# Kernel optimization log

Hardware: AMD Instinct MI355X
Metric: run time of the kernel (lower is better)

Reference implementation:

```python
import jax, jax.numpy as jnp
import numpy as np


def _lstm_cell(x, h, c, Wih, Whh, b):
    # torch gate order: input, forget, cell(g), output
    gates = x @ Wih.T + h @ Whh.T + b  # [B, 4H]
    i, f, g, o = jnp.split(gates, 4, axis=-1)
    i = jax.nn.sigmoid(i)
    f = jax.nn.sigmoid(f)
    g = jnp.tanh(g)
    o = jax.nn.sigmoid(o)
    c = f * c + i * g
    return o * jnp.tanh(c), c


def setup_inputs() -> dict:
    key = jax.random.key(0)
    ks = jax.random.split(key, 20)
    B, Te, Td, X, H = 4096, 168, 24, 8, 64
    s = 0.1  # weight scale for numerical sanity in the AR sampling loop
    return {
        "enc_x": jax.random.normal(ks[0], (B, Te, X), jnp.float32),
        "enc_z": jax.random.uniform(ks[1], (B, Te, 1), jnp.float32),
        "dec_x": jax.random.normal(ks[2], (B, Td, X - 1), jnp.float32),
        "v": jax.random.uniform(ks[3], (B, 1, 1), jnp.float32) + 0.5,  # positive scale
        "eps": jax.random.normal(ks[4], (B, Td, 1), jnp.float32),
        "W_ih0": s * jax.random.normal(ks[5], (4 * H, X), jnp.float32),
        "W_hh0": s * jax.random.normal(ks[6], (4 * H, H), jnp.float32),
        "b0": s * jax.random.normal(ks[7], (4 * H,), jnp.float32),
        "W_ih1": s * jax.random.normal(ks[8], (4 * H, H), jnp.float32),
        "W_hh1": s * jax.random.normal(ks[9], (4 * H, H), jnp.float32),
        "b1": s * jax.random.normal(ks[10], (4 * H,), jnp.float32),
        "W_ih2": s * jax.random.normal(ks[11], (4 * H, H), jnp.float32),
        "W_hh2": s * jax.random.normal(ks[12], (4 * H, H), jnp.float32),
        "b2": s * jax.random.normal(ks[13], (4 * H,), jnp.float32),
        "w_m": s * jax.random.normal(ks[14], (H, 1), jnp.float32),
        "b_m": jnp.zeros((1,), jnp.float32),
        "w_a": s * jax.random.normal(ks[15], (H, 1), jnp.float32),
        "b_a": jnp.zeros((1,), jnp.float32),
    }


def reference(enc_x, enc_z, dec_x, v, eps,
              W_ih0, W_hh0, b0, W_ih1, W_hh1, b1, W_ih2, W_hh2, b2,
              w_m, b_m, w_a, b_a):
    B = enc_x.shape[0]
    H = W_hh0.shape[1]

    def step3(x, h, c):
        h0, c0 = _lstm_cell(x, h[0], c[0], W_ih0, W_hh0, b0)
        h1, c1 = _lstm_cell(h0, h[1], c[1], W_ih1, W_hh1, b1)
        h2, c2 = _lstm_cell(h1, h[2], c[2], W_ih2, W_hh2, b2)
        return (h0, h1, h2), (c0, c1, c2), h2

    z0 = jnp.zeros((B, H), enc_x.dtype)
    h = (z0, z0, z0)
    c = (z0, z0, z0)

    # ---- encoder: 3-layer LSTM over Te steps ----
    def enc_step(carry, x_t):
        h, c = carry
        h, c, _ = step3(x_t, h, c)
        return (h, c), None

    (h, c), _ = jax.lax.scan(enc_step, (h, c), jnp.swapaxes(enc_x, 0, 1))

    vf = v[:, 0, :]                 # [B, 1]
    z = enc_z[:, -1, :] / vf        # [B, 1]

    def dec_step(carry, inp):
        h, c, z = carry
        x_t, e_t = inp              # [B, X-1], [B, 1]
        x = jnp.concatenate([z, x_t], axis=-1)   # [B, X]
        h, c, o = step3(x, h, c)
        m = (o @ w_m + b_m) * vf                  # Gaussian mean, rescaled
        a = jax.nn.softplus(o @ w_a + b_a) * vf   # Gaussian std, rescaled
        zs = m + a * e_t                          # reparameterized sample
        return (h, c, zs / vf), zs

    xs = (jnp.swapaxes(dec_x, 0, 1), jnp.swapaxes(eps, 0, 1))
    _, Z = jax.lax.scan(dec_step, (h, c, z), xs)  # [Td, B, 1]
    return jnp.swapaxes(Z, 0, 1)                  # [B, Td, 1]
```

## Files before the change

### kernel.cpp

```cpp
#include <hip/hip_runtime.h>
#include <math.h>

#define B_TOT 4096
#define TE 168
#define TD 24
#define NWG 256
#define HSTR 72
#define NB 4

typedef _Float16 f16;
typedef __attribute__((ext_vector_type(8))) _Float16 f16x8;
typedef __attribute__((ext_vector_type(4))) float f32x4;

#define SCL_S (-1.4426950408889634f)
#define SCL_G (2.885390081777927f)

__global__ __launch_bounds__(256) void pack_kernel(
    const float* __restrict__ Wih0, const float* __restrict__ Whh0,
    const float* __restrict__ Wih1, const float* __restrict__ Whh1,
    const float* __restrict__ Wih2, const float* __restrict__ Whh2,
    f16* __restrict__ pk)
{
    int idx = blockIdx.x * 256 + threadIdx.x;
    int j = idx & 7;
    int t = idx >> 3;
    int ln = t & 63; t >>= 6;
    int c  = t & 3;  t >>= 2;
    int q  = t & 3;  t >>= 2;
    int l  = t % 3;
    int w  = t / 3;
    int row = q * 64 + w * 16 + (ln & 15);
    int k   = c * 32 + ((ln >> 4) << 3) + j;
    float val = 0.f;
    if (l == 0) {
        if (k < 8)                 val = Wih0[row * 8 + k];
        else if (k >= 32 && k < 96) val = Whh0[row * 64 + (k - 32)];
    } else if (l == 1) {
        val = (k < 64) ? Wih1[row * 64 + k] : Whh1[row * 64 + (k - 64)];
    } else {
        val = (k < 64) ? Wih2[row * 64 + k] : Whh2[row * 64 + (k - 64)];
    }
    const float sc = (q == 2) ? SCL_G : SCL_S;
    pk[idx] = (f16)(val * sc);
}

__device__ __forceinline__ float softplusf(float x) { return fmaxf(x, 0.f) + log1pf(__expf(-fabsf(x))); }

__device__ __forceinline__ void wait_ge(volatile int* c, int tgt, int& seen) {
    if (seen < tgt) {
        int v;
        do { v = *c; } while (v < tgt);
        seen = v;
        asm volatile("" ::: "memory");
    }
}

__global__ __launch_bounds__(768, 3) void lstm_kernel(
    const float* __restrict__ enc_x, const float* __restrict__ enc_z,
    const float* __restrict__ dec_x, const float* __restrict__ v,
    const float* __restrict__ eps,   const f16* __restrict__ pk,
    const float* __restrict__ b0, const float* __restrict__ b1,
    const float* __restrict__ b2,
    const float* __restrict__ w_m, const float* __restrict__ b_m,
    const float* __restrict__ w_a, const float* __restrict__ b_a,
    float* __restrict__ out)
{
    const int tid  = threadIdx.x;
    const int lane = tid & 63;
    const int wv   = (tid >> 6) & 3;
    const int role = tid >> 8;
    const int bg   = blockIdx.x * 16;
    const int m16  = lane & 15;
    const int quad = lane >> 4;

    __shared__ f16   hbuf[NB][3][16][HSTR];
    __shared__ f16   xbuf[2][16][32];
    __shared__ float zbuf[16];
    __shared__ int   cnt[3];

    {
        uint* hz = (uint*)&hbuf[0][0][0][0];
        const int HW = NB * 3 * 16 * HSTR / 2;
        for (int i = tid; i < HW; i += 768) hz[i] = 0u;
        uint* xz = (uint*)&xbuf[0][0][0];
        for (int i = tid; i < 512; i += 768) xz[i] = 0u;
        if (tid < 3) cnt[tid] = 0;
    }

    f16x8 wgt[4][4];
#define PKOFF(l, q, c) ((((((size_t)wv * 3 + (l)) * 4 + (q)) * 4 + (c)) * 64 + lane) * 8)
    {
        const f16* pkr = pk + PKOFF(role, 0, 0);
#pragma unroll
        for (int q = 0; q < 4; ++q)
#pragma unroll
            for (int c = 0; c < 4; ++c)
                wgt[c][q] = *(const f16x8*)(pkr + (q * 4 + c) * 64 * 8);
    }
#undef PKOFF

    const int hid_self = wv * 16 + m16;
    f32x4 bsp[4];
    {
        const float* bp = (role == 0) ? b0 : (role == 1) ? b1 : b2;
#pragma unroll
        for (int q = 0; q < 4; ++q) {
            const float sc = (q == 2) ? SCL_G : SCL_S;
            float bv = bp[q * 64 + hid_self] * sc;
            bsp[q] = (f32x4){bv, bv, bv, bv};
        }
    }

    f16* hb = &hbuf[0][0][0][0];
    const int aoff = m16 * HSTR + quad * 8;
    float cst[4] = {};

#define HBASE(bf, l) (hb + ((bf) * 3 + (l)) * (16 * HSTR))
#define MFMA16(af, bf, cf) __builtin_amdgcn_mfma_f32_16x16x32_f16(af, bf, cf, 0, 0, 0)

#define MM_R(P, areg, wi)                                                     \
    {                                                                         \
        P##0 = MFMA16(areg, wgt[wi][0], bsp[0]);                              \
        P##1 = MFMA16(areg, wgt[wi][1], bsp[1]);                              \
        P##2 = MFMA16(areg, wgt[wi][2], bsp[2]);                              \
        P##3 = MFMA16(areg, wgt[wi][3], bsp[3]);                              \
    }
#define MM_F(P, aptr, wi)                                                     \
    {                                                                         \
        f16x8 af = *(const f16x8*)(aptr);                                     \
        P##0 = MFMA16(af, wgt[wi][0], bsp[0]);                                \
        P##1 = MFMA16(af, wgt[wi][1], bsp[1]);                                \
        P##2 = MFMA16(af, wgt[wi][2], bsp[2]);                                \
        P##3 = MFMA16(af, wgt[wi][3], bsp[3]);                                \
    }
#define MM(P, aptr, wi)                                                       \
    {                                                                         \
        f16x8 af = *(const f16x8*)(aptr);                                     \
        P##0 = MFMA16(af, wgt[wi][0], P##0);                                  \
        P##1 = MFMA16(af, wgt[wi][1], P##1);                                  \
        P##2 = MFMA16(af, wgt[wi][2], P##2);                                  \
        P##3 = MFMA16(af, wgt[wi][3], P##3);                                  \
    }

#define CELL(P, lh, BF)                                                       \
    {                                                                         \
        f16* hw = HBASE(BF, lh) + hid_self;                                   \
        _Pragma("unroll")                                                     \
        for (int r = 0; r < 4; ++r) {                                         \
            float Ei = __builtin_amdgcn_exp2f(P##0[r]);                       \
            float Ef = __builtin_amdgcn_exp2f(P##1[r]);                       \
            float Eg = __builtin_amdgcn_exp2f(P##2[r]);                       \
            float Eo = __builtin_amdgcn_exp2f(P##3[r]);                       \
            float ef1 = 1.f + Ef;                                             \
            float pig = (1.f + Ei) * (1.f + Eg);                              \
            float R   = __builtin_amdgcn_rcpf(pig * ef1);                     \
            float fv  = pig * R;                                              \
            float ig  = (Eg - 1.f) * ef1 * R;                                 \
            float cn  = fmaf(fv, cst[r], ig);                                 \
            cst[r] = cn;                                                      \
            float Ec  = __builtin_amdgcn_exp2f(cn * SCL_G);                   \
            float Roc = __builtin_amdgcn_rcpf((1.f + Eo) * (1.f + Ec));       \
            hw[(quad * 4 + r) * HSTR] = (f16)((Ec - 1.f) * Roc);              \
        }                                                                     \
    }

#define SIGNAL(i)                                                             \
    {                                                                         \
        asm volatile("s_waitcnt lgkmcnt(0)" ::: "memory");                    \
        atomicAdd((int*)&cnt[i], 1);                                          \
    }

    __syncthreads();

    if (role == 0) {
        const float* xp = enc_x + (size_t)(bg + m16) * (TE * 8);
        f32x4 xa = {}, xb = {};
        if (quad == 0) { xa = *(const f32x4*)xp; xb = *(const f32x4*)(xp + 4); }
        int s0 = 0, s1 = 0;
        for (int t = 0; t < TE; ++t) {
            wait_ge(&cnt[0], 4 * t, s0);
            wait_ge(&cnt[1], 4 * (t - (NB - 1)), s1);
            f16x8 af = {};
            if (quad == 0) {
#pragma unroll
                for (int j = 0; j < 4; ++j) { af[j] = (f16)xa[j]; af[4 + j] = (f16)xb[j]; }
                if (t + 1 < TE) {
                    xa = *(const f32x4*)(xp + (size_t)(t + 1) * 8);
                    xb = *(const f32x4*)(xp + (size_t)(t + 1) * 8 + 4);
                }
            }
            f32x4 a0, a1, a2, a3;
            MM_R(a, af, 0);
            const f16* h0p = HBASE((t + NB - 1) & (NB - 1), 0) + aoff;
            MM(a, h0p, 1);
            MM(a, h0p + 32, 2);
            CELL(a, 0, t & (NB - 1));
            SIGNAL(0);
        }
    } else if (role == 1) {
        int s0 = 0, s1 = 0, s2 = 0;
        for (int t = 0; t < TE; ++t) {
            wait_ge(&cnt[0], 4 * (t + 1), s0);
            wait_ge(&cnt[1], 4 * t, s1);
            wait_ge(&cnt[2], 4 * (t - (NB - 1)), s2);
            const f16* h0p = HBASE(t & (NB - 1), 0) + aoff;
            const f16* h1p = HBASE((t + NB - 1) & (NB - 1), 1) + aoff;
            f32x4 a0, a1, a2, a3;
            MM_F(a, h0p, 0);
            MM(a, h0p + 32, 1);
            MM(a, h1p, 2);
            MM(a, h1p + 32, 3);
            CELL(a, 1, t & (NB - 1));
            SIGNAL(1);
        }
    } else {
        int s1 = 0, s2 = 0;
        for (int t = 0; t < TE; ++t) {
            wait_ge(&cnt[1], 4 * (t + 1), s1);
            wait_ge(&cnt[2], 4 * t, s2);
            const f16* h1p = HBASE(t & (NB - 1), 1) + aoff;
            const f16* h2p = HBASE((t + NB - 1) & (NB - 1), 2) + aoff;
            f32x4 a0, a1, a2, a3;
            MM_F(a, h1p, 0);
            MM(a, h1p + 32, 1);
            MM(a, h2p, 2);
            MM(a, h2p + 32, 3);
            CELL(a, 2, t & (NB - 1));
            SIGNAL(2);
        }
    }

    __syncthreads();

    const int  sidx = tid - 512;
    const bool isst = (sidx >= 0) && (sidx < 128);
    const int  mS = (sidx >> 3) & 15, kS = sidx & 7;

    const int   mH = (tid >> 4) & 15;
    const float vf = (role == 0) ? v[bg + mH] : 0.f;
    float wmr[4], war[4];
#pragma unroll
    for (int r = 0; r < 4; ++r) {
        wmr[r] = w_m[(tid & 15) + 16 * r];
        war[r] = w_a[(tid & 15) + 16 * r];
    }
    const float bmv = b_m[0], bav = b_a[0];
    if (role == 0 && (tid & 15) == 0)
        zbuf[mH] = enc_z[(size_t)(bg + mH) * TE + (TE - 1)] / vf;

#define DEC_STEP(t)                                                           \
    {                                                                         \
        const int bc = (t) & (NB - 1);                                        \
        const int bp = ((t) + NB - 1) & (NB - 1);                             \
        __syncthreads();                           \
        if (isst) {                                                           \
            float xv = (kS == 0) ? zbuf[mS]                                   \
                                 : dec_x[((size_t)(bg + mS) * TD + (t)) * 7 + (kS - 1)]; \
            xbuf[(t) & 1][mS][kS] = (f16)xv;                                  \
        }                                                                     \
        __syncthreads();                                       \
        f32x4 a0, a1, a2, a3;                                                 \
        if (role == 0) {                                                      \
            MM_F(a, &xbuf[(t) & 1][0][0] + m16 * 32 + quad * 8, 0);           \
            MM(a, HBASE(bp, 0) + aoff,      1);                               \
            MM(a, HBASE(bp, 0) + aoff + 32, 2);                               \
            CELL(a, 0, bc);                                                   \
        }                                                                     \
        __syncthreads();                                      \
        if (role == 1) {                                                      \
            MM_F(a, HBASE(bc, 0) + aoff,      0);                             \
            MM(a, HBASE(bc, 0) + aoff + 32, 1);                               \
            MM(a, HBASE(bp, 1) + aoff,      2);                               \
            MM(a, HBASE(bp, 1) + aoff + 32, 3);                               \
            CELL(a, 1, bc);                                                   \
        }                                                                     \
        __syncthreads();                                      \
        if (role == 2) {                                                      \
            MM_F(a, HBASE(bc, 1) + aoff,      0);                             \
            MM(a, HBASE(bc, 1) + aoff + 32, 1);                               \
            MM(a, HBASE(bp, 2) + aoff,      2);                               \
            MM(a, HBASE(bp, 2) + aoff + 32, 3);                               \
            CELL(a, 2, bc);                                                   \
        }                                                                     \
        __syncthreads();                                      \
        if (role == 0) {                                                      \
            float sm = 0.f, sa = 0.f;                                         \
            const f16* h2p = HBASE(bc, 2) + mH * HSTR;                        \
            _Pragma("unroll")                                                 \
            for (int r = 0; r < 4; ++r) {                                     \
                float hv = (float)h2p[(tid & 15) + 16 * r];                   \
                sm += hv * wmr[r];                                            \
                sa += hv * war[r];                                            \
            }                                                                 \
            _Pragma("unroll")                                                 \
            for (int off = 1; off < 16; off <<= 1) {                          \
                sm += __shfl_xor(sm, off, 64);                                \
                sa += __shfl_xor(sa, off, 64);                                \
            }                                                                 \
            if ((tid & 15) == 0) {                                            \
                float mo  = (sm + bmv) * vf;                                  \
                float ao  = softplusf(sa + bav) * vf;                         \
                float zsv = mo + ao * eps[(size_t)(bg + mH) * TD + (t)];      \
                out[(size_t)(bg + mH) * TD + (t)] = zsv;                      \
                zbuf[mH] = zsv / vf;                                          \
            }                                                                 \
        }                                                                     \
    }

    for (int t = 0; t < TD; ++t) {
        DEC_STEP(t)
    }

#undef HBASE
#undef MFMA16
#undef MM_R
#undef MM_F
#undef MM
#undef CELL
#undef SIGNAL
#undef DEC_STEP
}

extern "C" void kernel_launch(void* const* d_in, const int* in_sizes, int n_in,
                              void* d_out, int out_size, void* d_ws, size_t ws_size,
                              hipStream_t stream) {
    const float* enc_x = (const float*)d_in[0];
    const float* enc_z = (const float*)d_in[1];
    const float* dec_x = (const float*)d_in[2];
    const float* v     = (const float*)d_in[3];
    const float* eps   = (const float*)d_in[4];
    const float* Wih0  = (const float*)d_in[5];
    const float* Whh0  = (const float*)d_in[6];
    const float* b0    = (const float*)d_in[7];
    const float* Wih1  = (const float*)d_in[8];
    const float* Whh1  = (const float*)d_in[9];
    const float* b1    = (const float*)d_in[10];
    const float* Wih2  = (const float*)d_in[11];
    const float* Whh2  = (const float*)d_in[12];
    const float* b2    = (const float*)d_in[13];
    const float* w_m   = (const float*)d_in[14];
    const float* b_m   = (const float*)d_in[15];
    const float* w_a   = (const float*)d_in[16];
    const float* b_a   = (const float*)d_in[17];
    float* out = (float*)d_out;
    f16*   pk  = (f16*)d_ws;

    pack_kernel<<<384, 256, 0, stream>>>(Wih0, Whh0, Wih1, Whh1, Wih2, Whh2, pk);
    lstm_kernel<<<NWG, 768, 0, stream>>>(enc_x, enc_z, dec_x, v, eps, pk,
                                         b0, b1, b2, w_m, b_m, w_a, b_a, out);
}
```

Baseline: 325.4 us.

## Replace LDS-atomic spin-wait pipelining with barrier-synchronized wavefront rounds

Swaps the encoder's per-layer spin-waits on LDS counters, which ran over a 4-deep ring buffer, for a skewed wavefront schedule. In each round all three layer groups compute different timesteps in parallel, separated by a single workgroup barrier and ping-pong double buffering. This removes polling on LDS atomics and the counter traffic, at the cost of a full barrier every step. The decoder is also streamlined: the staging pass through xbuf is dropped, x is built in registers, dec_x and eps are prefetched, and s_barrier is used instead of __syncthreads.

```diff
diff --git a/kernel.cpp b/kernel.cpp
--- a/kernel.cpp
+++ b/kernel.cpp
@@ -6,7 +6,6 @@
 #define TD 24
 #define NWG 256
 #define HSTR 72
-#define NB 4
 
 typedef _Float16 f16;
 typedef __attribute__((ext_vector_type(8))) _Float16 f16x8;
@@ -46,15 +45,6 @@
 
 __device__ __forceinline__ float softplusf(float x) { return fmaxf(x, 0.f) + log1pf(__expf(-fabsf(x))); }
 
-__device__ __forceinline__ void wait_ge(volatile int* c, int tgt, int& seen) {
-    if (seen < tgt) {
-        int v;
-        do { v = *c; } while (v < tgt);
-        seen = v;
-        asm volatile("" ::: "memory");
-    }
-}
-
 __global__ __launch_bounds__(768, 3) void lstm_kernel(
     const float* __restrict__ enc_x, const float* __restrict__ enc_z,
     const float* __restrict__ dec_x, const float* __restrict__ v,
@@ -73,18 +63,13 @@
     const int m16  = lane & 15;
     const int quad = lane >> 4;
 
-    __shared__ f16   hbuf[NB][3][16][HSTR];
-    __shared__ f16   xbuf[2][16][32];
+    __shared__ f16   hbuf[2][3][16][HSTR];
     __shared__ float zbuf[16];
-    __shared__ int   cnt[3];
 
     {
         uint* hz = (uint*)&hbuf[0][0][0][0];
-        const int HW = NB * 3 * 16 * HSTR / 2;
+        const int HW = 2 * 3 * 16 * HSTR / 2;
         for (int i = tid; i < HW; i += 768) hz[i] = 0u;
-        uint* xz = (uint*)&xbuf[0][0][0];
-        for (int i = tid; i < 512; i += 768) xz[i] = 0u;
-        if (tid < 3) cnt[tid] = 0;
     }
 
     f16x8 wgt[4][4];
@@ -115,7 +100,14 @@
     const int aoff = m16 * HSTR + quad * 8;
     float cst[4] = {};
 
-#define HBASE(bf, l) (hb + ((bf) * 3 + (l)) * (16 * HSTR))
+#define RBAR                                                                  \
+    {                                                                         \
+        asm volatile("s_waitcnt lgkmcnt(0)" ::: "memory");                    \
+        __builtin_amdgcn_s_barrier();                                         \
+        asm volatile("" ::: "memory");                                        \
+    }
+
+#define HBASE(pp, l) (hb + ((pp) * 3 + (l)) * (16 * HSTR))
 #define MFMA16(af, bf, cf) __builtin_amdgcn_mfma_f32_16x16x32_f16(af, bf, cf, 0, 0, 0)
 
 #define MM_R(P, areg, wi)                                                     \
@@ -142,9 +134,9 @@
         P##3 = MFMA16(af, wgt[wi][3], P##3);                                  \
     }
 
-#define CELL(P, lh, BF)                                                       \
-    {                                                                         \
-        f16* hw = HBASE(BF, lh) + hid_self;                                   \
+#define CELL(P, lh, PP)                                                       \
+    {                                                                         \
+        f16* hw = HBASE(PP, lh) + hid_self;                                   \
         _Pragma("unroll")                                                     \
         for (int r = 0; r < 4; ++r) {                                         \
             float Ei = __builtin_amdgcn_exp2f(P##0[r]);                       \
@@ -164,77 +156,64 @@
         }                                                                     \
     }
 
-#define SIGNAL(i)                                                             \
-    {                                                                         \
-        asm volatile("s_waitcnt lgkmcnt(0)" ::: "memory");                    \
-        atomicAdd((int*)&cnt[i], 1);                                          \
-    }
-
-    __syncthreads();
-
-    if (role == 0) {
-        const float* xp = enc_x + (size_t)(bg + m16) * (TE * 8);
-        f32x4 xa = {}, xb = {};
-        if (quad == 0) { xa = *(const f32x4*)xp; xb = *(const f32x4*)(xp + 4); }
-        int s0 = 0, s1 = 0;
-        for (int t = 0; t < TE; ++t) {
-            wait_ge(&cnt[0], 4 * t, s0);
-            wait_ge(&cnt[1], 4 * (t - (NB - 1)), s1);
-            f16x8 af = {};
-            if (quad == 0) {
-#pragma unroll
-                for (int j = 0; j < 4; ++j) { af[j] = (f16)xa[j]; af[4 + j] = (f16)xb[j]; }
-                if (t + 1 < TE) {
-                    xa = *(const f32x4*)(xp + (size_t)(t + 1) * 8);
-                    xb = *(const f32x4*)(xp + (size_t)(t + 1) * 8 + 4);
-                }
-            }
-            f32x4 a0, a1, a2, a3;
-            MM_R(a, af, 0);
-            const f16* h0p = HBASE((t + NB - 1) & (NB - 1), 0) + aoff;
-            MM(a, h0p, 1);
-            MM(a, h0p + 32, 2);
-            CELL(a, 0, t & (NB - 1));
-            SIGNAL(0);
-        }
-    } else if (role == 1) {
-        int s0 = 0, s1 = 0, s2 = 0;
-        for (int t = 0; t < TE; ++t) {
-            wait_ge(&cnt[0], 4 * (t + 1), s0);
-            wait_ge(&cnt[1], 4 * t, s1);
-            wait_ge(&cnt[2], 4 * (t - (NB - 1)), s2);
-            const f16* h0p = HBASE(t & (NB - 1), 0) + aoff;
-            const f16* h1p = HBASE((t + NB - 1) & (NB - 1), 1) + aoff;
-            f32x4 a0, a1, a2, a3;
-            MM_F(a, h0p, 0);
-            MM(a, h0p + 32, 1);
-            MM(a, h1p, 2);
-            MM(a, h1p + 32, 3);
-            CELL(a, 1, t & (NB - 1));
-            SIGNAL(1);
-        }
-    } else {
-        int s1 = 0, s2 = 0;
-        for (int t = 0; t < TE; ++t) {
-            wait_ge(&cnt[1], 4 * (t + 1), s1);
-            wait_ge(&cnt[2], 4 * t, s2);
-            const f16* h1p = HBASE(t & (NB - 1), 1) + aoff;
-            const f16* h2p = HBASE((t + NB - 1) & (NB - 1), 2) + aoff;
-            f32x4 a0, a1, a2, a3;
-            MM_F(a, h1p, 0);
-            MM(a, h1p + 32, 1);
-            MM(a, h2p, 2);
-            MM(a, h2p + 32, 3);
-            CELL(a, 2, t & (NB - 1));
-            SIGNAL(2);
-        }
-    }
-
-    __syncthreads();
-
-    const int  sidx = tid - 512;
-    const bool isst = (sidx >= 0) && (sidx < 128);
-    const int  mS = (sidx >> 3) & 15, kS = sidx & 7;
+    const float* xp = enc_x + (size_t)(bg + m16) * (TE * 8);
+    f32x4 xa = {}, xb = {};
+    if (role == 0) { xa = *(const f32x4*)xp; xb = *(const f32x4*)(xp + 4); }
+
+#define ROUND(PP, D0, D1, D2, T0)                                             \
+    {                                                                         \
+        RBAR;                                                                 \
+        f32x4 a0, a1, a2, a3;                                                 \
+        if (role == 0) {                                                      \
+            if (D0) {                                                         \
+                f16x8 af;                                                     \
+                _Pragma("unroll")                                             \
+                for (int j = 0; j < 4; ++j) {                                 \
+                    af[j] = (f16)xa[j]; af[4 + j] = (f16)xb[j];               \
+                }                                                             \
+                if ((T0) + 1 < TE) {                                          \
+                    xa = *(const f32x4*)(xp + (size_t)((T0) + 1) * 8);        \
+                    xb = *(const f32x4*)(xp + (size_t)((T0) + 1) * 8 + 4);    \
+                }                                                             \
+                MM_R(a, af, 0);                                               \
+                const f16* h0p = HBASE(1 - (PP), 0) + aoff;                   \
+                MM(a, h0p, 1);                                                \
+                MM(a, h0p + 32, 2);                                           \
+                CELL(a, 0, PP);                                               \
+            }                                                                 \
+        } else if (role == 1) {                                               \
+            if (D1) {                                                         \
+                const f16* h0p = HBASE(1 - (PP), 0) + aoff;                   \
+                const f16* h1p = HBASE(1 - (PP), 1) + aoff;                   \
+                MM_F(a, h0p, 0);                                              \
+                MM(a, h0p + 32, 1);                                           \
+                MM(a, h1p, 2);                                                \
+                MM(a, h1p + 32, 3);                                           \
+                CELL(a, 1, PP);                                               \
+            }                                                                 \
+        } else {                                                              \
+            if (D2) {                                                         \
+                const f16* h1p = HBASE(1 - (PP), 1) + aoff;                   \
+                const f16* h2p = HBASE(1 - (PP), 2) + aoff;                   \
+                MM_F(a, h1p, 0);                                              \
+                MM(a, h1p + 32, 1);                                           \
+                MM(a, h2p, 2);                                                \
+                MM(a, h2p + 32, 3);                                           \
+                CELL(a, 2, PP);                                               \
+            }                                                                 \
+        }                                                                     \
+    }
+
+    ROUND(0, 1, 0, 0, 0)
+    ROUND(1, 1, 1, 0, 1)
+    for (int t = 2; t < 166; t += 2) {
+        ROUND(0, 1, 1, 1, t)
+        ROUND(1, 1, 1, 1, t + 1)
+    }
+    ROUND(0, 1, 1, 1, 166)
+    ROUND(1, 1, 1, 1, 167)
+    ROUND(0, 0, 1, 1, 168)
+    ROUND(1, 0, 0, 1, 169)
 
     const int   mH = (tid >> 4) & 15;
     const float vf = (role == 0) ? v[bg + mH] : 0.f;
@@ -248,77 +227,97 @@
     if (role == 0 && (tid & 15) == 0)
         zbuf[mH] = enc_z[(size_t)(bg + mH) * TE + (TE - 1)] / vf;
 
-#define DEC_STEP(t)                                                           \
-    {                                                                         \
-        const int bc = (t) & (NB - 1);                                        \
-        const int bp = ((t) + NB - 1) & (NB - 1);                             \
-        __syncthreads();                           \
-        if (isst) {                                                           \
-            float xv = (kS == 0) ? zbuf[mS]                                   \
-                                 : dec_x[((size_t)(bg + mS) * TD + (t)) * 7 + (kS - 1)]; \
-            xbuf[(t) & 1][mS][kS] = (f16)xv;                                  \
-        }                                                                     \
-        __syncthreads();                                       \
-        f32x4 a0, a1, a2, a3;                                                 \
-        if (role == 0) {                                                      \
-            MM_F(a, &xbuf[(t) & 1][0][0] + m16 * 32 + quad * 8, 0);           \
-            MM(a, HBASE(bp, 0) + aoff,      1);                               \
-            MM(a, HBASE(bp, 0) + aoff + 32, 2);                               \
-            CELL(a, 0, bc);                                                   \
-        }                                                                     \
-        __syncthreads();                                      \
-        if (role == 1) {                                                      \
-            MM_F(a, HBASE(bc, 0) + aoff,      0);                             \
-            MM(a, HBASE(bc, 0) + aoff + 32, 1);                               \
-            MM(a, HBASE(bp, 1) + aoff,      2);                               \
-            MM(a, HBASE(bp, 1) + aoff + 32, 3);                               \
-            CELL(a, 1, bc);                                                   \
-        }                                                                     \
-        __syncthreads();                                      \
-        if (role == 2) {                                                      \
-            MM_F(a, HBASE(bc, 1) + aoff,      0);                             \
-            MM(a, HBASE(bc, 1) + aoff + 32, 1);                               \
-            MM(a, HBASE(bp, 2) + aoff,      2);                               \
-            MM(a, HBASE(bp, 2) + aoff + 32, 3);                               \
-            CELL(a, 2, bc);                                                   \
-        }                                                                     \
-        __syncthreads();                                      \
-        if (role == 0) {                                                      \
-            float sm = 0.f, sa = 0.f;                                         \
-            const f16* h2p = HBASE(bc, 2) + mH * HSTR;                        \
-            _Pragma("unroll")                                                 \
-            for (int r = 0; r < 4; ++r) {                                     \
-                float hv = (float)h2p[(tid & 15) + 16 * r];                   \
-                sm += hv * wmr[r];                                            \
-                sa += hv * war[r];                                            \
-            }                                                                 \
-            _Pragma("unroll")                                                 \
-            for (int off = 1; off < 16; off <<= 1) {                          \
-                sm += __shfl_xor(sm, off, 64);                                \
-                sa += __shfl_xor(sa, off, 64);                                \
-            }                                                                 \
-            if ((tid & 15) == 0) {                                            \
-                float mo  = (sm + bmv) * vf;                                  \
-                float ao  = softplusf(sa + bav) * vf;                         \
-                float zsv = mo + ao * eps[(size_t)(bg + mH) * TD + (t)];      \
-                out[(size_t)(bg + mH) * TD + (t)] = zsv;                      \
-                zbuf[mH] = zsv / vf;                                          \
-            }                                                                 \
-        }                                                                     \
+    float dxr[7];
+    if (role == 0) {
+#pragma unroll
+        for (int j = 0; j < 7; ++j)
+            dxr[j] = dec_x[((size_t)(bg + m16) * TD + 0) * 7 + j];
     }
 
     for (int t = 0; t < TD; ++t) {
-        DEC_STEP(t)
-    }
-
+        const int PA = t & 1;
+        float ev = 0.f;
+        RBAR;
+        {
+            f32x4 a0, a1, a2, a3;
+            if (role == 0) {
+                float zq = zbuf[m16];
+                ev = eps[(size_t)(bg + mH) * TD + t];
+                f16x8 af;
+                af[0] = (f16)zq;
+#pragma unroll
+                for (int j = 0; j < 7; ++j) af[1 + j] = (f16)dxr[j];
+                if (t + 1 < TD) {
+#pragma unroll
+                    for (int j = 0; j < 7; ++j)
+                        dxr[j] = dec_x[((size_t)(bg + m16) * TD + (t + 1)) * 7 + j];
+                }
+                MM_R(a, af, 0);
+                const f16* h0p = HBASE(1 - PA, 0) + aoff;
+                MM(a, h0p, 1);
+                MM(a, h0p + 32, 2);
+                CELL(a, 0, PA);
+            }
+        }
+        RBAR;
+        {
+            f32x4 a0, a1, a2, a3;
+            if (role == 1) {
+                const f16* h0p = HBASE(PA, 0) + aoff;
+                const f16* h1p = HBASE(PA, 1) + aoff;
+                MM_F(a, h0p, 0);
+                MM(a, h0p + 32, 1);
+                MM(a, h1p, 2);
+                MM(a, h1p + 32, 3);
+                CELL(a, 1, 1 - PA);
+            }
+        }
+        RBAR;
+        {
+            f32x4 a0, a1, a2, a3;
+            if (role == 2) {
+                const f16* h1p = HBASE(1 - PA, 1) + aoff;
+                const f16* h2p = HBASE(1 - PA, 2) + aoff;
+                MM_F(a, h1p, 0);
+                MM(a, h1p + 32, 1);
+                MM(a, h2p, 2);
+                MM(a, h2p + 32, 3);
+                CELL(a, 2, PA);
+            }
+        }
+        RBAR;
+        if (role == 0) {
+            float sm = 0.f, sa = 0.f;
+            const f16* h2p = HBASE(PA, 2) + mH * HSTR;
+#pragma unroll
+            for (int r = 0; r < 4; ++r) {
+                float hv = (float)h2p[(tid & 15) + 16 * r];
+                sm += hv * wmr[r];
+                sa += hv * war[r];
+            }
+#pragma unroll
+            for (int off = 1; off < 16; off <<= 1) {
+                sm += __shfl_xor(sm, off, 64);
+                sa += __shfl_xor(sa, off, 64);
+            }
+            if ((tid & 15) == 0) {
+                float mo  = (sm + bmv) * vf;
+                float ao  = softplusf(sa + bav) * vf;
+                float zsv = mo + ao * ev;
+                out[(size_t)(bg + mH) * TD + t] = zsv;
+                zbuf[mH] = zsv / vf;
+            }
+        }
+    }
+
+#undef RBAR
 #undef HBASE
 #undef MFMA16
 #undef MM_R
 #undef MM_F
 #undef MM
 #undef CELL
-#undef SIGNAL
-#undef DEC_STEP
+#undef ROUND
 }
 
 extern "C" void kernel_launch(void* const* d_in, const int* in_sizes, int n_in,
```

Result: faster. 315.2 us (-3.1%).
